# Performance work log

Hardware: AMD Instinct MI355X
Metric: run time of the kernel (lower is better)

## Reference

```python
import jax, jax.numpy as jnp
import numpy as np

B, N, D = 32768, 256, 3


def setup_inputs() -> dict:
    key = jax.random.key(0)
    k1, k2 = jax.random.split(key)
    keypoints = jax.random.normal(k1, (B, N, D), dtype=jnp.float32)
    perm = jax.random.permutation(k2, B)  # emulates torch.randperm, deterministic
    return {"keypoints": keypoints, "perm": perm}


def _transform_a2b(src, dst):
    # src, dst: [B, N, 3]; batched similarity (Umeyama/Kabsch-style) alignment.
    num = src.shape[1]
    src_mean = src.mean(axis=1)                     # [B, 3]
    dst_mean = dst.mean(axis=1)                     # [B, 3]
    src_d = src - src_mean[:, None]                 # [B, N, 3]
    dst_d = dst - dst_mean[:, None]                 # [B, N, 3]
    A = jnp.einsum('bni,bnj->bij', dst_d, src_d) / num  # [B, 3, 3] covariance
    U, S, Vt = jnp.linalg.svd(A)
    # NOTE: in the original torch code `d[neg_A][:, -1, -1] = -1` writes into a
    # COPY (advanced indexing), so d stays identity for all batches. We
    # faithfully reproduce that actual behavior: R = U @ V^T, scale uses sum(S).
    var_sum = jnp.mean(jnp.sum(src_d * src_d, axis=-1), axis=1)  # sum of per-dim biased var
    scale = jnp.sum(S, axis=-1) / var_sum           # [B]
    R = U @ Vt                                      # [B, 3, 3]
    T = dst_mean - scale[:, None] * jnp.einsum('bij,bj->bi', R, src_mean)  # [B, 3]
    # Original computes R, scale, T under torch.no_grad().
    R = jax.lax.stop_gradient(R)
    scale = jax.lax.stop_gradient(scale)
    T = jax.lax.stop_gradient(T)
    return src @ (jnp.swapaxes(R, -1, -2) * scale[:, None, None]) + T[:, None]


def reference(keypoints, perm):
    dst = keypoints[perm]                            # randomized keypoints
    trans = _transform_a2b(keypoints, dst)
    return jnp.mean(jnp.abs(trans - dst))
```

## Files before the change

### kernel.cpp

```cpp
#include <hip/hip_runtime.h>
#include <math.h>

#define GEO_N 256

__device__ __forceinline__ float frcp(float x) { return __builtin_amdgcn_rcpf(x); }
__device__ __forceinline__ float frsq(float x) { return __builtin_amdgcn_rsqf(x); }
__device__ __forceinline__ float fsqrtf_(float x) { return __builtin_amdgcn_sqrtf(x); }

__device__ __forceinline__ float wredf(float v) {
#pragma unroll
  for (int off = 32; off; off >>= 1) v += __shfl_xor(v, off, 64);
  return v;
}

__device__ __forceinline__ float hred16(const float r[16], int lane) {
  float v8[8], v4[4], v2[2], v1;
  const int b1 = lane & 1, b2 = (lane >> 1) & 1, b3 = (lane >> 2) & 1, b4 = (lane >> 3) & 1;
#pragma unroll
  for (int k = 0; k < 8; ++k) {
    float send = b1 ? r[k] : r[k + 8];
    float recv = __shfl_xor(send, 1, 64);
    v8[k] = (b1 ? r[k + 8] : r[k]) + recv;
  }
#pragma unroll
  for (int k = 0; k < 4; ++k) {
    float send = b2 ? v8[k] : v8[k + 4];
    float recv = __shfl_xor(send, 2, 64);
    v4[k] = (b2 ? v8[k + 4] : v8[k]) + recv;
  }
#pragma unroll
  for (int k = 0; k < 2; ++k) {
    float send = b3 ? v4[k] : v4[k + 2];
    float recv = __shfl_xor(send, 4, 64);
    v2[k] = (b3 ? v4[k + 2] : v4[k]) + recv;
  }
  {
    float send = b4 ? v2[0] : v2[1];
    float recv = __shfl_xor(send, 8, 64);
    v1 = (b4 ? v2[1] : v2[0]) + recv;
  }
  v1 += __shfl_xor(v1, 16, 64);
  v1 += __shfl_xor(v1, 32, 64);
  return v1;
}

template <int P, int Q>
__device__ __forceinline__ void jrot(float G[3][3], float V[3][3]) {
  const float apq = G[P][Q];
  const float tau = (G[Q][Q] - G[P][P]) * 0.5f * frcp(apq);
  const float tt = fsqrtf_(1.0f + tau * tau);
  const float tr = frcp(tau + copysignf(tt, tau));
  const float cr = frsq(1.0f + tr * tr);
  const bool skip = fabsf(apq) < 1e-30f;
  const float c = skip ? 1.0f : cr;
  const float s = skip ? 0.0f : tr * cr;
#pragma unroll
  for (int k = 0; k < 3; ++k) {
    float gkp = G[k][P], gkq = G[k][Q];
    G[k][P] = c * gkp - s * gkq;
    G[k][Q] = s * gkp + c * gkq;
  }
#pragma unroll
  for (int k = 0; k < 3; ++k) {
    float gpk = G[P][k], gqk = G[Q][k];
    G[P][k] = c * gpk - s * gqk;
    G[Q][k] = s * gpk + c * gqk;
  }
#pragma unroll
  for (int k = 0; k < 3; ++k) {
    float vkp = V[k][P], vkq = V[k][Q];
    V[k][P] = c * vkp - s * vkq;
    V[k][Q] = s * vkp + c * vkq;
  }
}

__device__ __forceinline__ void solve_rst(const float s0[16], float bc[13]) {
  const float invN = 1.0f / (float)GEO_N;
  const float smx = s0[0] * invN, smy = s0[1] * invN, smz = s0[2] * invN;
  const float dmx = s0[3] * invN, dmy = s0[4] * invN, dmz = s0[5] * invN;
  float A[3][3];
  A[0][0] = s0[6] * invN - dmx * smx;  A[0][1] = s0[7] * invN - dmx * smy;  A[0][2] = s0[8] * invN - dmx * smz;
  A[1][0] = s0[9] * invN - dmy * smx;  A[1][1] = s0[10] * invN - dmy * smy; A[1][2] = s0[11] * invN - dmy * smz;
  A[2][0] = s0[12] * invN - dmz * smx; A[2][1] = s0[13] * invN - dmz * smy; A[2][2] = s0[14] * invN - dmz * smz;
  const float var_sum = s0[15] * invN - (smx * smx + smy * smy + smz * smz);

  float G[3][3];
#pragma unroll
  for (int i = 0; i < 3; ++i)
#pragma unroll
    for (int j = 0; j < 3; ++j)
      G[i][j] = A[0][i] * A[0][j] + A[1][i] * A[1][j] + A[2][i] * A[2][j];
  float V[3][3] = {{1, 0, 0}, {0, 1, 0}, {0, 0, 1}};
#pragma unroll
  for (int sweep = 0; sweep < 4; ++sweep) {
    jrot<0, 1>(G, V);
    jrot<0, 2>(G, V);
    jrot<1, 2>(G, V);
  }
  float l0 = G[0][0], l1 = G[1][1], l2 = G[2][2];
  if (l0 < l1) { float tl = l0; l0 = l1; l1 = tl;
#pragma unroll
    for (int k = 0; k < 3; ++k) { float tv = V[k][0]; V[k][0] = V[k][1]; V[k][1] = tv; } }
  if (l0 < l2) { float tl = l0; l0 = l2; l2 = tl;
#pragma unroll
    for (int k = 0; k < 3; ++k) { float tv = V[k][0]; V[k][0] = V[k][2]; V[k][2] = tv; } }
  if (l1 < l2) { float tl = l1; l1 = l2; l2 = tl;
#pragma unroll
    for (int k = 0; k < 3; ++k) { float tv = V[k][1]; V[k][1] = V[k][2]; V[k][2] = tv; } }
  const float sig0 = fsqrtf_(fmaxf(l0, 0.0f));
  const float sig1 = fsqrtf_(fmaxf(l1, 0.0f));
  const float sig2 = fsqrtf_(fmaxf(l2, 0.0f));

  float v0[3] = {V[0][0], V[1][0], V[2][0]};
  float v1[3] = {V[0][1], V[1][1], V[2][1]};
  float v2[3] = {V[0][2], V[1][2], V[2][2]};
  float u0[3], u1[3], u2r[3];
#pragma unroll
  for (int i = 0; i < 3; ++i) {
    u0[i]  = A[i][0] * v0[0] + A[i][1] * v0[1] + A[i][2] * v0[2];
    u1[i]  = A[i][0] * v1[0] + A[i][1] * v1[1] + A[i][2] * v1[2];
    u2r[i] = A[i][0] * v2[0] + A[i][1] * v2[1] + A[i][2] * v2[2];
  }
  float n0 = u0[0] * u0[0] + u0[1] * u0[1] + u0[2] * u0[2];
  if (n0 > 1e-28f) { float inv = frsq(n0); u0[0] *= inv; u0[1] *= inv; u0[2] *= inv; }
  else { u0[0] = 1.0f; u0[1] = 0.0f; u0[2] = 0.0f; }
  float d01 = u1[0] * u0[0] + u1[1] * u0[1] + u1[2] * u0[2];
  u1[0] -= d01 * u0[0]; u1[1] -= d01 * u0[1]; u1[2] -= d01 * u0[2];
  float n1 = u1[0] * u1[0] + u1[1] * u1[1] + u1[2] * u1[2];
  if (n1 > 1e-28f) { float inv = frsq(n1); u1[0] *= inv; u1[1] *= inv; u1[2] *= inv; }
  else {
    float ex[3] = {1, 0, 0}, ey[3] = {0, 1, 0};
    const float* e = (fabsf(u0[0]) < 0.9f) ? ex : ey;
    u1[0] = u0[1] * e[2] - u0[2] * e[1];
    u1[1] = u0[2] * e[0] - u0[0] * e[2];
    u1[2] = u0[0] * e[1] - u0[1] * e[0];
    float nn = u1[0] * u1[0] + u1[1] * u1[1] + u1[2] * u1[2];
    float inv = frsq(nn);
    u1[0] *= inv; u1[1] *= inv; u1[2] *= inv;
  }
  float u2[3] = {u0[1] * u1[2] - u0[2] * u1[1],
                 u0[2] * u1[0] - u0[0] * u1[2],
                 u0[0] * u1[1] - u0[1] * u1[0]};
  float d2 = u2[0] * u2r[0] + u2[1] * u2r[1] + u2[2] * u2r[2];
  if (d2 < 0.0f) { u2[0] = -u2[0]; u2[1] = -u2[1]; u2[2] = -u2[2]; }

  const float scale = (sig0 + sig1 + sig2) * frcp(fmaxf(var_sum, 1e-30f));
  float R[3][3];
#pragma unroll
  for (int i = 0; i < 3; ++i)
#pragma unroll
    for (int j = 0; j < 3; ++j)
      R[i][j] = u0[i] * v0[j] + u1[i] * v1[j] + u2[i] * v2[j];
  const float Tx = dmx - scale * (R[0][0] * smx + R[0][1] * smy + R[0][2] * smz);
  const float Ty = dmy - scale * (R[1][0] * smx + R[1][1] * smy + R[1][2] * smz);
  const float Tz = dmz - scale * (R[2][0] * smx + R[2][1] * smy + R[2][2] * smz);
#pragma unroll
  for (int i = 0; i < 3; ++i)
#pragma unroll
    for (int j = 0; j < 3; ++j) bc[3 * i + j] = R[i][j];
  bc[9] = scale; bc[10] = Tx; bc[11] = Ty; bc[12] = Tz;
}

__global__ __launch_bounds__(256) void geo_wave4(const float* __restrict__ kp,
                                                 const int* __restrict__ perm,
                                                 float* __restrict__ partials,
                                                 int B, int NW) {
  const int wid = (blockIdx.x << 2) | (threadIdx.x >> 6);
  if (wid >= NW) return;
  const int lane = threadIdx.x & 63;
  const int b0 = wid * 4;
  const float4* base = (const float4*)kp;

  int pm[4];
#pragma unroll
  for (int i = 0; i < 4; ++i) pm[i] = perm[min(b0 + i, B - 1)];

  float4 S[4][3], D[4][3];
#pragma unroll
  for (int i = 0; i < 4; ++i) {
    const int bb = min(b0 + i, B - 1);
    const float4* s4 = base + (size_t)bb * 192 + lane * 3;
    const float4* d4 = base + (size_t)pm[i] * 192 + lane * 3;
    S[i][0] = s4[0]; S[i][1] = s4[1]; S[i][2] = s4[2];
    D[i][0] = d4[0]; D[i][1] = d4[1]; D[i][2] = d4[2];
  }

  float parked = 0.0f;
#pragma unroll
  for (int i = 0; i < 4; ++i) {
    const float s[12] = {S[i][0].x, S[i][0].y, S[i][0].z, S[i][0].w,
                         S[i][1].x, S[i][1].y, S[i][1].z, S[i][1].w,
                         S[i][2].x, S[i][2].y, S[i][2].z, S[i][2].w};
    const float d[12] = {D[i][0].x, D[i][0].y, D[i][0].z, D[i][0].w,
                         D[i][1].x, D[i][1].y, D[i][1].z, D[i][1].w,
                         D[i][2].x, D[i][2].y, D[i][2].z, D[i][2].w};
    float r[16];
#pragma unroll
    for (int k = 0; k < 16; ++k) r[k] = 0.0f;
#pragma unroll
    for (int p = 0; p < 4; ++p) {
      const float sx = s[3 * p + 0], sy = s[3 * p + 1], sz = s[3 * p + 2];
      const float dx = d[3 * p + 0], dy = d[3 * p + 1], dz = d[3 * p + 2];
      r[0] += sx; r[1] += sy; r[2] += sz;
      r[3] += dx; r[4] += dy; r[5] += dz;
      r[6] += dx * sx; r[7] += dx * sy; r[8] += dx * sz;
      r[9] += dy * sx; r[10] += dy * sy; r[11] += dy * sz;
      r[12] += dz * sx; r[13] += dz * sy; r[14] += dz * sz;
      r[15] += sx * sx + sy * sy + sz * sz;
    }
    const float v = hred16(r, lane);
    if ((lane >> 4) == i) parked = v;
  }

  constexpr int br[16] = {0, 8, 4, 12, 2, 10, 6, 14, 1, 9, 5, 13, 3, 11, 7, 15};
  float s0[16];
#pragma unroll
  for (int k = 0; k < 16; ++k)
    s0[k] = __shfl(parked, ((lane & 3) << 4) | br[k], 64);

  float bc[13];
  solve_rst(s0, bc);

  float acc = 0.0f;
#pragma unroll
  for (int i = 0; i < 4; ++i) {
    const float R00 = __shfl(bc[0], i, 64), R01 = __shfl(bc[1], i, 64), R02 = __shfl(bc[2], i, 64);
    const float R10 = __shfl(bc[3], i, 64), R11 = __shfl(bc[4], i, 64), R12 = __shfl(bc[5], i, 64);
    const float R20 = __shfl(bc[6], i, 64), R21 = __shfl(bc[7], i, 64), R22 = __shfl(bc[8], i, 64);
    const float sc  = __shfl(bc[9], i, 64);
    const float Tx  = __shfl(bc[10], i, 64), Ty = __shfl(bc[11], i, 64), Tz = __shfl(bc[12], i, 64);
    const float s[12] = {S[i][0].x, S[i][0].y, S[i][0].z, S[i][0].w,
                         S[i][1].x, S[i][1].y, S[i][1].z, S[i][1].w,
                         S[i][2].x, S[i][2].y, S[i][2].z, S[i][2].w};
    const float d[12] = {D[i][0].x, D[i][0].y, D[i][0].z, D[i][0].w,
                         D[i][1].x, D[i][1].y, D[i][1].z, D[i][1].w,
                         D[i][2].x, D[i][2].y, D[i][2].z, D[i][2].w};
    float a = 0.0f;
#pragma unroll
    for (int q = 0; q < 4; ++q) {
      const float sx = s[3 * q + 0], sy = s[3 * q + 1], sz = s[3 * q + 2];
      const float dx = d[3 * q + 0], dy = d[3 * q + 1], dz = d[3 * q + 2];
      const float e0 = sc * (R00 * sx + R01 * sy + R02 * sz) + Tx - dx;
      const float e1 = sc * (R10 * sx + R11 * sy + R12 * sz) + Ty - dy;
      const float e2 = sc * (R20 * sx + R21 * sy + R22 * sz) + Tz - dz;
      a += fabsf(e0) + fabsf(e1) + fabsf(e2);
    }
    if (b0 + i < B) acc += a;
  }
  acc = wredf(acc);
  if (lane == 0) partials[wid] = acc;
}

__global__ __launch_bounds__(1024) void geo_fin(const float* __restrict__ partials,
                                                float* __restrict__ out, int n,
                                                double inv_total) {
  const int t = threadIdx.x;
  double acc = 0.0;
  for (int i = t; i < n; i += 1024) acc += (double)partials[i];
#pragma unroll
  for (int off = 32; off; off >>= 1) acc += __shfl_xor(acc, off, 64);
  __shared__ double sred[16];
  if ((t & 63) == 0) sred[t >> 6] = acc;
  __syncthreads();
  if (t == 0) {
    double tot = 0.0;
#pragma unroll
    for (int k = 0; k < 16; ++k) tot += sred[k];
    out[0] = (float)(tot * inv_total);
  }
}

extern "C" void kernel_launch(void* const* d_in, const int* in_sizes, int n_in,
                              void* d_out, int out_size, void* d_ws, size_t ws_size,
                              hipStream_t stream) {
  const float* kp = (const float*)d_in[0];
  const int* perm = (const int*)d_in[1];
  float* out = (float*)d_out;
  const int B = in_sizes[1];
  const double inv_total = 1.0 / ((double)B * (double)GEO_N * 3.0);

  const int NW = (B + 3) / 4;
  float* partials = (float*)d_ws;
  const int grid = (NW + 3) / 4;
  geo_wave4<<<grid, 256, 0, stream>>>(kp, perm, partials, B, NW);
  geo_fin<<<1, 1024, 0, stream>>>(partials, out, NW, inv_total);
}
```

Measured before the change: 45.17 us.

## Map each 16-lane group to one batch instead of interleaving four batches per wave

Each wave previously loaded all four batches across its 64 lanes, reduced them one at a time and shuffled the solved transforms back to every lane. Now each 16-lane quarter owns one batch: each lane loads 12 contiguous float4s for source and destination, the reduction runs once within the 16-lane group, and each lane applies its own group's solved transform with no broadcast shuffles. This removes three of the four reduction passes and all transform broadcast shuffles. The cost is higher register pressure (96 floats of inputs per lane) and less coalesced loads, since each lane now reads 192 contiguous bytes.

```diff
diff --git a/kernel.cpp b/kernel.cpp
--- a/kernel.cpp
+++ b/kernel.cpp
@@ -11,37 +11,6 @@
 #pragma unroll
   for (int off = 32; off; off >>= 1) v += __shfl_xor(v, off, 64);
   return v;
-}
-
-__device__ __forceinline__ float hred16(const float r[16], int lane) {
-  float v8[8], v4[4], v2[2], v1;
-  const int b1 = lane & 1, b2 = (lane >> 1) & 1, b3 = (lane >> 2) & 1, b4 = (lane >> 3) & 1;
-#pragma unroll
-  for (int k = 0; k < 8; ++k) {
-    float send = b1 ? r[k] : r[k + 8];
-    float recv = __shfl_xor(send, 1, 64);
-    v8[k] = (b1 ? r[k + 8] : r[k]) + recv;
-  }
-#pragma unroll
-  for (int k = 0; k < 4; ++k) {
-    float send = b2 ? v8[k] : v8[k + 4];
-    float recv = __shfl_xor(send, 2, 64);
-    v4[k] = (b2 ? v8[k + 4] : v8[k]) + recv;
-  }
-#pragma unroll
-  for (int k = 0; k < 2; ++k) {
-    float send = b3 ? v4[k] : v4[k + 2];
-    float recv = __shfl_xor(send, 4, 64);
-    v2[k] = (b3 ? v4[k + 2] : v4[k]) + recv;
-  }
-  {
-    float send = b4 ? v2[0] : v2[1];
-    float recv = __shfl_xor(send, 8, 64);
-    v1 = (b4 ? v2[1] : v2[0]) + recv;
-  }
-  v1 += __shfl_xor(v1, 16, 64);
-  v1 += __shfl_xor(v1, 32, 64);
-  return v1;
 }
 
 template <int P, int Q>
@@ -161,92 +130,98 @@
   bc[9] = scale; bc[10] = Tx; bc[11] = Ty; bc[12] = Tz;
 }
 
-__global__ __launch_bounds__(256) void geo_wave4(const float* __restrict__ kp,
-                                                 const int* __restrict__ perm,
-                                                 float* __restrict__ partials,
-                                                 int B, int NW) {
+__global__ __launch_bounds__(256) void geo_wave4t(const float* __restrict__ kp,
+                                                  const int* __restrict__ perm,
+                                                  float* __restrict__ partials,
+                                                  int B, int NW) {
   const int wid = (blockIdx.x << 2) | (threadIdx.x >> 6);
   if (wid >= NW) return;
   const int lane = threadIdx.x & 63;
+  const int g = lane >> 4, q = lane & 15;
   const int b0 = wid * 4;
+  const int bi = b0 + g;
+  const int bb = min(bi, B - 1);
   const float4* base = (const float4*)kp;
 
-  int pm[4];
-#pragma unroll
-  for (int i = 0; i < 4; ++i) pm[i] = perm[min(b0 + i, B - 1)];
-
-  float4 S[4][3], D[4][3];
-#pragma unroll
-  for (int i = 0; i < 4; ++i) {
-    const int bb = min(b0 + i, B - 1);
-    const float4* s4 = base + (size_t)bb * 192 + lane * 3;
-    const float4* d4 = base + (size_t)pm[i] * 192 + lane * 3;
-    S[i][0] = s4[0]; S[i][1] = s4[1]; S[i][2] = s4[2];
-    D[i][0] = d4[0]; D[i][1] = d4[1]; D[i][2] = d4[2];
-  }
-
-  float parked = 0.0f;
-#pragma unroll
-  for (int i = 0; i < 4; ++i) {
-    const float s[12] = {S[i][0].x, S[i][0].y, S[i][0].z, S[i][0].w,
-                         S[i][1].x, S[i][1].y, S[i][1].z, S[i][1].w,
-                         S[i][2].x, S[i][2].y, S[i][2].z, S[i][2].w};
-    const float d[12] = {D[i][0].x, D[i][0].y, D[i][0].z, D[i][0].w,
-                         D[i][1].x, D[i][1].y, D[i][1].z, D[i][1].w,
-                         D[i][2].x, D[i][2].y, D[i][2].z, D[i][2].w};
-    float r[16];
-#pragma unroll
-    for (int k = 0; k < 16; ++k) r[k] = 0.0f;
-#pragma unroll
-    for (int p = 0; p < 4; ++p) {
-      const float sx = s[3 * p + 0], sy = s[3 * p + 1], sz = s[3 * p + 2];
-      const float dx = d[3 * p + 0], dy = d[3 * p + 1], dz = d[3 * p + 2];
-      r[0] += sx; r[1] += sy; r[2] += sz;
-      r[3] += dx; r[4] += dy; r[5] += dz;
-      r[6] += dx * sx; r[7] += dx * sy; r[8] += dx * sz;
-      r[9] += dy * sx; r[10] += dy * sy; r[11] += dy * sz;
-      r[12] += dz * sx; r[13] += dz * sy; r[14] += dz * sz;
-      r[15] += sx * sx + sy * sy + sz * sz;
-    }
-    const float v = hred16(r, lane);
-    if ((lane >> 4) == i) parked = v;
+  const int pm = perm[bb];
+
+  const float4* s4 = base + (size_t)bb * 192 + q * 12;
+  const float4* d4 = base + (size_t)pm * 192 + q * 12;
+  float4 S[12], D[12];
+#pragma unroll
+  for (int j = 0; j < 12; ++j) S[j] = s4[j];
+#pragma unroll
+  for (int j = 0; j < 12; ++j) D[j] = d4[j];
+
+  float s[48], d[48];
+#pragma unroll
+  for (int j = 0; j < 12; ++j) {
+    s[4 * j + 0] = S[j].x; s[4 * j + 1] = S[j].y; s[4 * j + 2] = S[j].z; s[4 * j + 3] = S[j].w;
+    d[4 * j + 0] = D[j].x; d[4 * j + 1] = D[j].y; d[4 * j + 2] = D[j].z; d[4 * j + 3] = D[j].w;
+  }
+
+  float r[16];
+#pragma unroll
+  for (int k = 0; k < 16; ++k) r[k] = 0.0f;
+#pragma unroll
+  for (int p = 0; p < 16; ++p) {
+    const float sx = s[3 * p + 0], sy = s[3 * p + 1], sz = s[3 * p + 2];
+    const float dx = d[3 * p + 0], dy = d[3 * p + 1], dz = d[3 * p + 2];
+    r[0] += sx; r[1] += sy; r[2] += sz;
+    r[3] += dx; r[4] += dy; r[5] += dz;
+    r[6] += dx * sx; r[7] += dx * sy; r[8] += dx * sz;
+    r[9] += dy * sx; r[10] += dy * sy; r[11] += dy * sz;
+    r[12] += dz * sx; r[13] += dz * sy; r[14] += dz * sz;
+    r[15] += sx * sx + sy * sy + sz * sz;
+  }
+
+  const int b1 = q & 1, b2 = (q >> 1) & 1, b3 = (q >> 2) & 1, b4 = (q >> 3) & 1;
+  float v8[8], v4[4], v2[2], parked;
+#pragma unroll
+  for (int k = 0; k < 8; ++k) {
+    float send = b1 ? r[k] : r[k + 8];
+    float recv = __shfl_xor(send, 1, 64);
+    v8[k] = (b1 ? r[k + 8] : r[k]) + recv;
+  }
+#pragma unroll
+  for (int k = 0; k < 4; ++k) {
+    float send = b2 ? v8[k] : v8[k + 4];
+    float recv = __shfl_xor(send, 2, 64);
+    v4[k] = (b2 ? v8[k + 4] : v8[k]) + recv;
+  }
+#pragma unroll
+  for (int k = 0; k < 2; ++k) {
+    float send = b3 ? v4[k] : v4[k + 2];
+    float recv = __shfl_xor(send, 4, 64);
+    v2[k] = (b3 ? v4[k + 2] : v4[k]) + recv;
+  }
+  {
+    float send = b4 ? v2[0] : v2[1];
+    float recv = __shfl_xor(send, 8, 64);
+    parked = (b4 ? v2[1] : v2[0]) + recv;
   }
 
   constexpr int br[16] = {0, 8, 4, 12, 2, 10, 6, 14, 1, 9, 5, 13, 3, 11, 7, 15};
   float s0[16];
 #pragma unroll
   for (int k = 0; k < 16; ++k)
-    s0[k] = __shfl(parked, ((lane & 3) << 4) | br[k], 64);
+    s0[k] = __shfl(parked, (lane & 0x30) | br[k], 64);
 
   float bc[13];
   solve_rst(s0, bc);
 
   float acc = 0.0f;
 #pragma unroll
-  for (int i = 0; i < 4; ++i) {
-    const float R00 = __shfl(bc[0], i, 64), R01 = __shfl(bc[1], i, 64), R02 = __shfl(bc[2], i, 64);
-    const float R10 = __shfl(bc[3], i, 64), R11 = __shfl(bc[4], i, 64), R12 = __shfl(bc[5], i, 64);
-    const float R20 = __shfl(bc[6], i, 64), R21 = __shfl(bc[7], i, 64), R22 = __shfl(bc[8], i, 64);
-    const float sc  = __shfl(bc[9], i, 64);
-    const float Tx  = __shfl(bc[10], i, 64), Ty = __shfl(bc[11], i, 64), Tz = __shfl(bc[12], i, 64);
-    const float s[12] = {S[i][0].x, S[i][0].y, S[i][0].z, S[i][0].w,
-                         S[i][1].x, S[i][1].y, S[i][1].z, S[i][1].w,
-                         S[i][2].x, S[i][2].y, S[i][2].z, S[i][2].w};
-    const float d[12] = {D[i][0].x, D[i][0].y, D[i][0].z, D[i][0].w,
-                         D[i][1].x, D[i][1].y, D[i][1].z, D[i][1].w,
-                         D[i][2].x, D[i][2].y, D[i][2].z, D[i][2].w};
-    float a = 0.0f;
-#pragma unroll
-    for (int q = 0; q < 4; ++q) {
-      const float sx = s[3 * q + 0], sy = s[3 * q + 1], sz = s[3 * q + 2];
-      const float dx = d[3 * q + 0], dy = d[3 * q + 1], dz = d[3 * q + 2];
-      const float e0 = sc * (R00 * sx + R01 * sy + R02 * sz) + Tx - dx;
-      const float e1 = sc * (R10 * sx + R11 * sy + R12 * sz) + Ty - dy;
-      const float e2 = sc * (R20 * sx + R21 * sy + R22 * sz) + Tz - dz;
-      a += fabsf(e0) + fabsf(e1) + fabsf(e2);
-    }
-    if (b0 + i < B) acc += a;
-  }
+  for (int p = 0; p < 16; ++p) {
+    const float sx = s[3 * p + 0], sy = s[3 * p + 1], sz = s[3 * p + 2];
+    const float dx = d[3 * p + 0], dy = d[3 * p + 1], dz = d[3 * p + 2];
+    const float e0 = bc[9] * (bc[0] * sx + bc[1] * sy + bc[2] * sz) + bc[10] - dx;
+    const float e1 = bc[9] * (bc[3] * sx + bc[4] * sy + bc[5] * sz) + bc[11] - dy;
+    const float e2 = bc[9] * (bc[6] * sx + bc[7] * sy + bc[8] * sz) + bc[12] - dz;
+    acc += fabsf(e0) + fabsf(e1) + fabsf(e2);
+  }
+  if (bi >= B) acc = 0.0f;
+
   acc = wredf(acc);
   if (lane == 0) partials[wid] = acc;
 }
@@ -282,6 +257,6 @@
   const int NW = (B + 3) / 4;
   float* partials = (float*)d_ws;
   const int grid = (NW + 3) / 4;
-  geo_wave4<<<grid, 256, 0, stream>>>(kp, perm, partials, B, NW);
+  geo_wave4t<<<grid, 256, 0, stream>>>(kp, perm, partials, B, NW);
   geo_fin<<<1, 1024, 0, stream>>>(partials, out, NW, inv_total);
 }
```

Result: slower. 46.58 us (+3.1%).
